# Optimization experiments

Hardware: AMD Instinct MI355X
Metric: run time of the kernel (lower is better)

The kernel has to match this reference:

```python
import jax, jax.numpy as jnp
import numpy as np

D_MODEL = 1024
NUM_HEADS = 16
D_K = D_MODEL // NUM_HEADS


def setup_inputs() -> dict:
    key = jax.random.key(0)
    ks = jax.random.split(key, 5)
    sd = np.sqrt(2.0 / (D_MODEL + D_MODEL))
    x = jax.random.normal(ks[0], (2, 2048, D_MODEL), dtype=jnp.float32)
    # weights stored as [out_features, in_features] like torch Linear
    w_q = jax.random.normal(ks[1], (D_MODEL, D_MODEL), dtype=jnp.float32) * (sd * sd)
    w_k = jax.random.normal(ks[2], (D_MODEL, D_MODEL), dtype=jnp.float32) * (sd * sd)
    w_v = jax.random.normal(ks[3], (D_MODEL, D_MODEL), dtype=jnp.float32) * (sd * sd)
    w_o = jax.random.normal(ks[4], (D_MODEL, D_MODEL), dtype=jnp.float32) * (sd * sd)
    return {"x": x, "w_q": w_q, "w_k": w_k, "w_v": w_v, "w_o": w_o}


def reference(x, w_q, w_k, w_v, w_o):
    B, S, D = x.shape
    H, Dk = NUM_HEADS, D_K
    # projections: x @ W.T
    q = (x @ w_q.T).reshape(B, S, H, Dk).transpose(0, 2, 1, 3)  # [B,H,S,Dk]
    k = (x @ w_k.T).reshape(B, S, H, Dk).transpose(0, 2, 1, 3)
    v = (x @ w_v.T).reshape(B, S, H, Dk).transpose(0, 2, 1, 3)
    scale = 1.0 / np.sqrt(Dk).astype(np.float32)
    scores = jnp.einsum('bhqd,bhkd->bhqk', q, k) * scale  # [B,H,S,S]
    causal = jnp.tril(jnp.ones((S, S), dtype=bool))
    scores = jnp.where(causal, scores, -jnp.inf)
    weights = jax.nn.softmax(scores, axis=-1)
    attn = jnp.einsum('bhqk,bhkd->bhqd', weights, v)  # [B,H,S,Dk]
    attn = attn.transpose(0, 2, 1, 3).reshape(B, S, D)
    return attn @ w_o.T
```

## Files before the change

### kernel.cpp

```cpp
#include <hip/hip_runtime.h>

typedef __attribute__((ext_vector_type(8))) short short8;
typedef __attribute__((ext_vector_type(4))) float f32x4;
typedef __attribute__((ext_vector_type(16))) float f32x16;
typedef __attribute__((ext_vector_type(2))) unsigned int u32x2;

#define DM 1024
#define SL 2048
#define NH 16
#define DKH 64
#define NB 2

__device__ __forceinline__ unsigned short f2bf(float f) {
    union { float f; unsigned int u; } a; a.f = f;
    unsigned int r = a.u + 0x7FFFu + ((a.u >> 16) & 1u);
    return (unsigned short)(r >> 16);
}

__device__ __forceinline__ void gl_lds16(const void* g, void* l) {
    __builtin_amdgcn_global_load_lds(
        (__attribute__((address_space(1))) void*)(g),
        (__attribute__((address_space(3))) void*)(l), 16, 0, 0);
}

__device__ __forceinline__ unsigned int cvtpk_bf16(float lo, float hi) {
    unsigned int r;
    asm("v_cvt_pk_bf16_f32 %0, %1, %2" : "=v"(r) : "v"(lo), "v"(hi));
    return r;
}

__device__ __forceinline__ void pl32swap(unsigned int &a, unsigned int &b) {
    u32x2 r = __builtin_amdgcn_permlane32_swap(a, b, false, false);
    a = r[0]; b = r[1];
}
__device__ __forceinline__ void pl32swapf(float &a, float &b) {
    unsigned int ua = __float_as_uint(a), ub = __float_as_uint(b);
    pl32swap(ua, ub);
    a = __uint_as_float(ua); b = __uint_as_float(ub);
}

__global__ __launch_bounds__(256) void convert_kernel(
    const float* __restrict__ x,  const float* __restrict__ wq,
    const float* __restrict__ wk, const float* __restrict__ wv,
    const float* __restrict__ wo,
    unsigned short* __restrict__ xb,  unsigned short* __restrict__ wqb,
    unsigned short* __restrict__ wkb, unsigned short* __restrict__ wvb,
    unsigned short* __restrict__ wob)
{
    const int NX = NB * SL * DM;
    const int NW = DM * DM;
    int t4 = (blockIdx.x * 256 + threadIdx.x) * 4;
    const float* src; unsigned short* dst; int off; float scale = 1.0f;
    if (t4 < NX)              { src = x;  dst = xb;  off = t4; }
    else if (t4 < NX + NW)    { src = wq; dst = wqb; off = t4 - NX; scale = 0.125f * 1.44269504088896f; }
    else if (t4 < NX + 2*NW)  { src = wk; dst = wkb; off = t4 - NX - NW; }
    else if (t4 < NX + 3*NW)  { src = wv; dst = wvb; off = t4 - NX - 2*NW; }
    else                      { src = wo; dst = wob; off = t4 - NX - 3*NW; }
    float4 v = *(const float4*)(src + off);
    unsigned long long p =
        (unsigned long long)f2bf(v.x * scale)
      | ((unsigned long long)f2bf(v.y * scale) << 16)
      | ((unsigned long long)f2bf(v.z * scale) << 32)
      | ((unsigned long long)f2bf(v.w * scale) << 48);
    *(unsigned long long*)(dst + off) = p;
}

template<int MODE>
__global__ __launch_bounds__(256) void gemm_bt(
    const unsigned short* __restrict__ A,
    const unsigned short* __restrict__ Bw,
    unsigned short* __restrict__ oq, unsigned short* __restrict__ ok,
    unsigned short* __restrict__ ov, float* __restrict__ of)
{
    __shared__ __align__(16) unsigned short As[128 * 64];
    __shared__ __align__(16) unsigned short Bs[128 * 64];
    const int tid  = threadIdx.x;
    const int lane = tid & 63;
    const int wave = tid >> 6;
    const int wm = (wave >> 1) * 64, wn = (wave & 1) * 64;
    const int bx = blockIdx.x, by = blockIdx.y;
    const int c    = lane & 15;
    const int kg16 = (lane >> 4) * 16;
    const int swz  = (c & 7) << 4;

    f32x4 acc[4][4];
    #pragma unroll
    for (int i = 0; i < 4; i++)
        #pragma unroll
        for (int j = 0; j < 4; j++) acc[i][j] = (f32x4){0.f, 0.f, 0.f, 0.f};

    const char* Ab = (const char*)A  + by * 128 * (DM * 2);
    const char* Bb = (const char*)Bw + bx * 128 * (DM * 2);

    for (int k0 = 0; k0 < DM; k0 += 64) {
        #pragma unroll
        for (int i = 0; i < 4; i++) {
            int o  = i * 4096 + tid * 16;
            int r  = o >> 7;
            int cb = o & 127;
            int src = r * (DM * 2) + k0 * 2 + (cb ^ ((r & 7) << 4));
            gl_lds16(Ab + src, (char*)As + o);
            gl_lds16(Bb + src, (char*)Bs + o);
        }
        __syncthreads();
        #pragma unroll
        for (int kk = 0; kk < 2; kk++) {
            short8 a[4], bfr[4];
            #pragma unroll
            for (int mi = 0; mi < 4; mi++)
                a[mi] = *(const short8*)((const char*)As
                        + (wm + mi * 16 + c) * 128 + ((kk * 64 + kg16) ^ swz));
            #pragma unroll
            for (int ni = 0; ni < 4; ni++)
                bfr[ni] = *(const short8*)((const char*)Bs
                        + (wn + ni * 16 + c) * 128 + ((kk * 64 + kg16) ^ swz));
            #pragma unroll
            for (int mi = 0; mi < 4; mi++)
                #pragma unroll
                for (int ni = 0; ni < 4; ni++)
                    acc[mi][ni] = __builtin_amdgcn_mfma_f32_16x16x32_bf16(
                        a[mi], bfr[ni], acc[mi][ni], 0, 0, 0);
        }
        __syncthreads();
    }

    const int r4 = (lane >> 4) * 4;
    if (MODE == 0) {
        const int mat = (bx * 128) >> 10;
        unsigned short* outb = (mat == 0) ? oq : (mat == 1) ? ok : ov;
        const int nb = bx * 128 - (mat << 10);
        #pragma unroll
        for (int mi = 0; mi < 4; mi++) {
            int m_g = by * 128 + wm + mi * 16 + r4;
            int b_  = m_g >> 11, s_ = m_g & 2047;
            #pragma unroll
            for (int ni = 0; ni < 4; ni++) {
                int n_l = nb + wn + ni * 16 + c;
                int h = n_l >> 6, dk = n_l & 63;
                #pragma unroll
                for (int j = 0; j < 4; j++)
                    outb[((b_ * NH + h) * SL + (s_ + j)) * DKH + dk] = f2bf(acc[mi][ni][j]);
            }
        }
    } else {
        #pragma unroll
        for (int mi = 0; mi < 4; mi++) {
            int m_g = by * 128 + wm + mi * 16 + r4;
            #pragma unroll
            for (int ni = 0; ni < 4; ni++) {
                int n_g = bx * 128 + wn + ni * 16 + c;
                #pragma unroll
                for (int j = 0; j < 4; j++)
                    of[(m_g + j) * DM + n_g] = acc[mi][ni][j];
            }
        }
    }
}

__global__ __launch_bounds__(256) void attn_kernel(
    const unsigned short* __restrict__ Q,
    const unsigned short* __restrict__ K,
    const unsigned short* __restrict__ V,
    unsigned short* __restrict__ O)
{
    __shared__ __align__(16) unsigned short Kl[2][128 * 64];
    __shared__ __align__(16) unsigned short Vt[2][16 * 64 * 8];
    const int tid = threadIdx.x, lane = tid & 63, wave = tid >> 6;
    const int ln31 = lane & 31, hi = lane >> 5;
    const int qt_raw = blockIdx.x >> 5;
    const int bh     = blockIdx.x & 31;
    const int qt = qt_raw < 8 ? qt_raw : 23 - qt_raw;
    const int b = bh >> 4, h = bh & 15;
    const int bhi = b * NH + h;
    const unsigned short* Qg = Q + bhi * (SL * DKH);
    const unsigned short* Kg = K + bhi * (SL * DKH);
    const unsigned short* Vg = V + bhi * (SL * DKH);
    const int qw = qt * 128 + wave * 32;
    const int ntiles = qt + 1;
    const int vd0 = (tid & 31) * 2, c0 = tid >> 5;

    short8 qf[4];
    #pragma unroll
    for (int ks = 0; ks < 4; ks++)
        qf[ks] = *(const short8*)&Qg[(qw + ln31) * DKH + ks * 16 + hi * 8];

    f32x16 OT0, OT1;
    #pragma unroll
    for (int r = 0; r < 16; r++) { OT0[r] = 0.f; OT1[r] = 0.f; }
    float mrun = -1e30f, ls = 0.f;

    unsigned int vreg[16];

    #pragma unroll
    for (int i = 0; i < 4; i++) {
        int s = i * 256 + tid;
        int kv = s >> 3;
        int k8 = (s & 7) ^ (kv & 7);
        gl_lds16((const char*)Kg + kv * 128 + k8 * 16, (char*)&Kl[0][0] + s * 16);
    }
    #pragma unroll
    for (int c2 = 0; c2 < 2; c2++)
        #pragma unroll
        for (int i = 0; i < 8; i++)
            vreg[c2 * 8 + i] = *(const unsigned int*)&Vg[((c0 + c2 * 8) * 8 + i) * DKH + vd0];

    for (int t = 0; t < ntiles; ++t) {
        const int buf = t & 1;
        const int kv0 = t * 128;
        #pragma unroll
        for (int c2 = 0; c2 < 2; c2++) {
            int chunk = c0 + c2 * 8;
            short8 sa, sb;
            #pragma unroll
            for (int i = 0; i < 8; i++) {
                unsigned int pr = vreg[c2 * 8 + i];
                sa[i] = (short)(pr & 0xFFFFu);
                sb[i] = (short)(pr >> 16);
            }
            *(short8*)&Vt[buf][(chunk * 64 + vd0) * 8]     = sa;
            *(short8*)&Vt[buf][(chunk * 64 + vd0 + 1) * 8] = sb;
        }
        __syncthreads();

        if (t + 1 < ntiles) {
            const int kv1 = (t + 1) * 128;
            #pragma unroll
            for (int i = 0; i < 4; i++) {
                int s = i * 256 + tid;
                int kv = s >> 3;
                int k8 = (s & 7) ^ (kv & 7);
                gl_lds16((const char*)Kg + (size_t)(kv1 + kv) * 128 + k8 * 16,
                         (char*)&Kl[buf ^ 1][0] + s * 16);
            }
            #pragma unroll
            for (int c2 = 0; c2 < 2; c2++)
                #pragma unroll
                for (int i = 0; i < 8; i++)
                    vreg[c2 * 8 + i] = *(const unsigned int*)&Vg[(size_t)(kv1 + (c0 + c2 * 8) * 8 + i) * DKH + vd0];
        }

        const char* kb = (const char*)&Kl[buf][0];
        const unsigned short* vb = &Vt[buf][0];
        #pragma unroll
        for (int hh = 0; hh < 2; hh++) {
            const int kvh = kv0 + hh * 64;
            if (kvh > qw + 31) break;

            f32x16 S0, S1;
            #pragma unroll
            for (int r = 0; r < 16; r++) { S0[r] = 0.f; S1[r] = 0.f; }
            #pragma unroll
            for (int ks = 0; ks < 4; ks++) {
                int ko = (ks * 32 + hi * 16) ^ ((ln31 & 7) << 4);
                short8 ka0 = *(const short8*)(kb + (hh * 64 + ln31) * 128 + ko);
                short8 ka1 = *(const short8*)(kb + (hh * 64 + 32 + ln31) * 128 + ko);
                S0 = __builtin_amdgcn_mfma_f32_32x32x16_bf16(ka0, qf[ks], S0, 0, 0, 0);
                S1 = __builtin_amdgcn_mfma_f32_32x32x16_bf16(ka1, qf[ks], S1, 0, 0, 0);
            }

            if (kvh + 63 > qw) {
                const int qrel0 = qw + ln31 - kvh - 4 * hi;
                const int qrel1 = qrel0 - 32;
                #pragma unroll
                for (int r = 0; r < 16; r++) {
                    const int ro = (r & 3) + 8 * (r >> 2);
                    if (ro > qrel0) S0[r] = -1e30f;
                    if (ro > qrel1) S1[r] = -1e30f;
                }
            }

            float mx = fmaxf(S0[0], S1[0]);
            #pragma unroll
            for (int r = 1; r < 16; r++) mx = fmaxf(mx, fmaxf(S0[r], S1[r]));
            float ma = mx, mb = mx;
            pl32swapf(ma, mb);
            float rm = fmaxf(ma, mb);

            if (__any(rm > mrun + 8.f)) {
                float nm = fmaxf(mrun, rm);
                float corr = exp2f(mrun - nm);
                mrun = nm; ls *= corr;
                #pragma unroll
                for (int r = 0; r < 16; r++) { OT0[r] *= corr; OT1[r] *= corr; }
            }

            float psum = 0.f;
            #pragma unroll
            for (int r = 0; r < 16; r++) {
                S0[r] = exp2f(S0[r] - mrun); psum += S0[r];
                S1[r] = exp2f(S1[r] - mrun); psum += S1[r];
            }
            ls += psum;

            short8 pf[4];
            {
                unsigned int wa, wb, wc, wd;
                wa = cvtpk_bf16(S0[0], S0[1]);   wb = cvtpk_bf16(S0[4], S0[5]);
                pl32swap(wa, wb);
                wc = cvtpk_bf16(S0[2], S0[3]);   wd = cvtpk_bf16(S0[6], S0[7]);
                pl32swap(wc, wd);
                union { unsigned int u[4]; short8 s; } w0 = {{wa, wc, wb, wd}};
                pf[0] = w0.s;

                wa = cvtpk_bf16(S0[8], S0[9]);   wb = cvtpk_bf16(S0[12], S0[13]);
                pl32swap(wa, wb);
                wc = cvtpk_bf16(S0[10], S0[11]); wd = cvtpk_bf16(S0[14], S0[15]);
                pl32swap(wc, wd);
                union { unsigned int u[4]; short8 s; } w1 = {{wa, wc, wb, wd}};
                pf[1] = w1.s;

                wa = cvtpk_bf16(S1[0], S1[1]);   wb = cvtpk_bf16(S1[4], S1[5]);
                pl32swap(wa, wb);
                wc = cvtpk_bf16(S1[2], S1[3]);   wd = cvtpk_bf16(S1[6], S1[7]);
                pl32swap(wc, wd);
                union { unsigned int u[4]; short8 s; } w2 = {{wa, wc, wb, wd}};
                pf[2] = w2.s;

                wa = cvtpk_bf16(S1[8], S1[9]);   wb = cvtpk_bf16(S1[12], S1[13]);
                pl32swap(wa, wb);
                wc = cvtpk_bf16(S1[10], S1[11]); wd = cvtpk_bf16(S1[14], S1[15]);
                pl32swap(wc, wd);
                union { unsigned int u[4]; short8 s; } w3 = {{wa, wc, wb, wd}};
                pf[3] = w3.s;
            }

            #pragma unroll
            for (int ks2 = 0; ks2 < 4; ks2++) {
                int slot = (hh * 8 + ks2 * 2 + hi) * 64;
                short8 va0 = *(const short8*)&vb[(slot + ln31) * 8];
                short8 va1 = *(const short8*)&vb[(slot + 32 + ln31) * 8];
                OT0 = __builtin_amdgcn_mfma_f32_32x32x16_bf16(va0, pf[ks2], OT0, 0, 0, 0);
                OT1 = __builtin_amdgcn_mfma_f32_32x32x16_bf16(va1, pf[ks2], OT1, 0, 0, 0);
            }
        }
    }

    float la = ls, lb = ls;
    pl32swapf(la, lb);
    float inv = 1.0f / (la + lb);
    const int qrow = qw + ln31;
    const size_t base = (size_t)(b * SL + qrow) * DM + h * DKH;
    #pragma unroll
    for (int r = 0; r < 16; r++) {
        const int d0 = (r & 3) + 8 * (r >> 2) + 4 * hi;
        O[base + d0]      = f2bf(OT0[r] * inv);
        O[base + 32 + d0] = f2bf(OT1[r] * inv);
    }
}

extern "C" void kernel_launch(void* const* d_in, const int* in_sizes, int n_in,
                              void* d_out, int out_size, void* d_ws, size_t ws_size,
                              hipStream_t stream)
{
    const float* x  = (const float*)d_in[0];
    const float* wq = (const float*)d_in[1];
    const float* wk = (const float*)d_in[2];
    const float* wv = (const float*)d_in[3];
    const float* wo = (const float*)d_in[4];
    char* ws = (char*)d_ws;
    unsigned short* xb  = (unsigned short*)(ws);
    unsigned short* wqb = (unsigned short*)(ws + (8ll  << 20));
    unsigned short* wkb = (unsigned short*)(ws + (10ll << 20));
    unsigned short* wvb = (unsigned short*)(ws + (12ll << 20));
    unsigned short* wob = (unsigned short*)(ws + (14ll << 20));
    unsigned short* Qb  = (unsigned short*)(ws + (16ll << 20));
    unsigned short* Kb  = (unsigned short*)(ws + (24ll << 20));
    unsigned short* Vb  = (unsigned short*)(ws + (32ll << 20));
    unsigned short* Abf = (unsigned short*)(ws + (40ll << 20));
    float* out = (float*)d_out;

    convert_kernel<<<dim3(8192), dim3(256), 0, stream>>>(
        x, wq, wk, wv, wo, xb, wqb, wkb, wvb, wob);

    gemm_bt<0><<<dim3(24, 32), dim3(256), 0, stream>>>(
        xb, wqb, Qb, Kb, Vb, (float*)nullptr);

    attn_kernel<<<dim3(512), dim3(256), 0, stream>>>(Qb, Kb, Vb, Abf);

    gemm_bt<1><<<dim3(8, 32), dim3(256), 0, stream>>>(
        Abf, wob, nullptr, nullptr, nullptr, out);
}
```

Before: 120.2 us.

## Shrink attention blocks to 64-query tiles with 2 waves and 64-key tiles

The attention kernel moves from 256-thread blocks covering 128 queries to 128-thread blocks covering 64 queries, with 64-key tiles, so the grid doubles to 1024 blocks. Causal load balancing becomes a four-way pairing of query tiles. The inner two-half loop goes away and only the final tile is masked. It also adds s_setprio around the MFMA sections and uses the raw exp2 builtin. The aim is better occupancy and load balance, at the cost of more K/V reloads across blocks and more barriers per unit of work.

```diff
diff --git a/kernel.cpp b/kernel.cpp
--- a/kernel.cpp
+++ b/kernel.cpp
@@ -157,25 +157,29 @@
     }
 }
 
-__global__ __launch_bounds__(256) void attn_kernel(
+__global__ __launch_bounds__(128) void attn_kernel(
     const unsigned short* __restrict__ Q,
     const unsigned short* __restrict__ K,
     const unsigned short* __restrict__ V,
     unsigned short* __restrict__ O)
 {
-    __shared__ __align__(16) unsigned short Kl[2][128 * 64];
-    __shared__ __align__(16) unsigned short Vt[2][16 * 64 * 8];
+    __shared__ __align__(16) unsigned short Kl[2][64 * 64];
+    __shared__ __align__(16) unsigned short Vt[2][8 * 64 * 8];
     const int tid = threadIdx.x, lane = tid & 63, wave = tid >> 6;
     const int ln31 = lane & 31, hi = lane >> 5;
     const int qt_raw = blockIdx.x >> 5;
     const int bh     = blockIdx.x & 31;
-    const int qt = qt_raw < 8 ? qt_raw : 23 - qt_raw;
+    const int quad = qt_raw >> 3;
+    const int qt = (quad == 0) ? qt_raw
+                 : (quad == 1) ? (23 - qt_raw)
+                 : (quad == 2) ? (qt_raw + 8)
+                 :               (47 - qt_raw);
     const int b = bh >> 4, h = bh & 15;
     const int bhi = b * NH + h;
     const unsigned short* Qg = Q + bhi * (SL * DKH);
     const unsigned short* Kg = K + bhi * (SL * DKH);
     const unsigned short* Vg = V + bhi * (SL * DKH);
-    const int qw = qt * 128 + wave * 32;
+    const int qw = qt * 64 + wave * 32;
     const int ntiles = qt + 1;
     const int vd0 = (tid & 31) * 2, c0 = tid >> 5;
 
@@ -193,7 +197,7 @@
 
     #pragma unroll
     for (int i = 0; i < 4; i++) {
-        int s = i * 256 + tid;
+        int s = i * 128 + tid;
         int kv = s >> 3;
         int k8 = (s & 7) ^ (kv & 7);
         gl_lds16((const char*)Kg + kv * 128 + k8 * 16, (char*)&Kl[0][0] + s * 16);
@@ -202,14 +206,14 @@
     for (int c2 = 0; c2 < 2; c2++)
         #pragma unroll
         for (int i = 0; i < 8; i++)
-            vreg[c2 * 8 + i] = *(const unsigned int*)&Vg[((c0 + c2 * 8) * 8 + i) * DKH + vd0];
+            vreg[c2 * 8 + i] = *(const unsigned int*)&Vg[((c0 + 4 * c2) * 8 + i) * DKH + vd0];
 
     for (int t = 0; t < ntiles; ++t) {
         const int buf = t & 1;
-        const int kv0 = t * 128;
+        const int kv0 = t * 64;
         #pragma unroll
         for (int c2 = 0; c2 < 2; c2++) {
-            int chunk = c0 + c2 * 8;
+            int chunk = c0 + 4 * c2;
             short8 sa, sb;
             #pragma unroll
             for (int i = 0; i < 8; i++) {
@@ -223,10 +227,10 @@
         __syncthreads();
 
         if (t + 1 < ntiles) {
-            const int kv1 = (t + 1) * 128;
+            const int kv1 = (t + 1) * 64;
             #pragma unroll
             for (int i = 0; i < 4; i++) {
-                int s = i * 256 + tid;
+                int s = i * 128 + tid;
                 int kv = s >> 3;
                 int k8 = (s & 7) ^ (kv & 7);
                 gl_lds16((const char*)Kg + (size_t)(kv1 + kv) * 128 + k8 * 16,
@@ -236,103 +240,102 @@
             for (int c2 = 0; c2 < 2; c2++)
                 #pragma unroll
                 for (int i = 0; i < 8; i++)
-                    vreg[c2 * 8 + i] = *(const unsigned int*)&Vg[(size_t)(kv1 + (c0 + c2 * 8) * 8 + i) * DKH + vd0];
+                    vreg[c2 * 8 + i] = *(const unsigned int*)&Vg[(size_t)(kv1 + (c0 + 4 * c2) * 8 + i) * DKH + vd0];
         }
 
         const char* kb = (const char*)&Kl[buf][0];
         const unsigned short* vb = &Vt[buf][0];
-        #pragma unroll
-        for (int hh = 0; hh < 2; hh++) {
-            const int kvh = kv0 + hh * 64;
-            if (kvh > qw + 31) break;
-
-            f32x16 S0, S1;
-            #pragma unroll
-            for (int r = 0; r < 16; r++) { S0[r] = 0.f; S1[r] = 0.f; }
-            #pragma unroll
-            for (int ks = 0; ks < 4; ks++) {
-                int ko = (ks * 32 + hi * 16) ^ ((ln31 & 7) << 4);
-                short8 ka0 = *(const short8*)(kb + (hh * 64 + ln31) * 128 + ko);
-                short8 ka1 = *(const short8*)(kb + (hh * 64 + 32 + ln31) * 128 + ko);
-                S0 = __builtin_amdgcn_mfma_f32_32x32x16_bf16(ka0, qf[ks], S0, 0, 0, 0);
-                S1 = __builtin_amdgcn_mfma_f32_32x32x16_bf16(ka1, qf[ks], S1, 0, 0, 0);
-            }
-
-            if (kvh + 63 > qw) {
-                const int qrel0 = qw + ln31 - kvh - 4 * hi;
-                const int qrel1 = qrel0 - 32;
-                #pragma unroll
-                for (int r = 0; r < 16; r++) {
-                    const int ro = (r & 3) + 8 * (r >> 2);
-                    if (ro > qrel0) S0[r] = -1e30f;
-                    if (ro > qrel1) S1[r] = -1e30f;
-                }
-            }
-
-            float mx = fmaxf(S0[0], S1[0]);
-            #pragma unroll
-            for (int r = 1; r < 16; r++) mx = fmaxf(mx, fmaxf(S0[r], S1[r]));
-            float ma = mx, mb = mx;
-            pl32swapf(ma, mb);
-            float rm = fmaxf(ma, mb);
-
-            if (__any(rm > mrun + 8.f)) {
-                float nm = fmaxf(mrun, rm);
-                float corr = exp2f(mrun - nm);
-                mrun = nm; ls *= corr;
-                #pragma unroll
-                for (int r = 0; r < 16; r++) { OT0[r] *= corr; OT1[r] *= corr; }
-            }
-
-            float psum = 0.f;
+
+        f32x16 S0, S1;
+        #pragma unroll
+        for (int r = 0; r < 16; r++) { S0[r] = 0.f; S1[r] = 0.f; }
+        __builtin_amdgcn_s_setprio(1);
+        #pragma unroll
+        for (int ks = 0; ks < 4; ks++) {
+            int ko = (ks * 32 + hi * 16) ^ ((ln31 & 7) << 4);
+            short8 ka0 = *(const short8*)(kb + ln31 * 128 + ko);
+            short8 ka1 = *(const short8*)(kb + (32 + ln31) * 128 + ko);
+            S0 = __builtin_amdgcn_mfma_f32_32x32x16_bf16(ka0, qf[ks], S0, 0, 0, 0);
+            S1 = __builtin_amdgcn_mfma_f32_32x32x16_bf16(ka1, qf[ks], S1, 0, 0, 0);
+        }
+        __builtin_amdgcn_s_setprio(0);
+
+        if (t == ntiles - 1) {
+            const int qrel0 = qw + ln31 - kv0 - 4 * hi;
+            const int qrel1 = qrel0 - 32;
             #pragma unroll
             for (int r = 0; r < 16; r++) {
-                S0[r] = exp2f(S0[r] - mrun); psum += S0[r];
-                S1[r] = exp2f(S1[r] - mrun); psum += S1[r];
-            }
-            ls += psum;
-
-            short8 pf[4];
-            {
-                unsigned int wa, wb, wc, wd;
-                wa = cvtpk_bf16(S0[0], S0[1]);   wb = cvtpk_bf16(S0[4], S0[5]);
-                pl32swap(wa, wb);
-                wc = cvtpk_bf16(S0[2], S0[3]);   wd = cvtpk_bf16(S0[6], S0[7]);
-                pl32swap(wc, wd);
-                union { unsigned int u[4]; short8 s; } w0 = {{wa, wc, wb, wd}};
-                pf[0] = w0.s;
-
-                wa = cvtpk_bf16(S0[8], S0[9]);   wb = cvtpk_bf16(S0[12], S0[13]);
-                pl32swap(wa, wb);
-                wc = cvtpk_bf16(S0[10], S0[11]); wd = cvtpk_bf16(S0[14], S0[15]);
-                pl32swap(wc, wd);
-                union { unsigned int u[4]; short8 s; } w1 = {{wa, wc, wb, wd}};
-                pf[1] = w1.s;
-
-                wa = cvtpk_bf16(S1[0], S1[1]);   wb = cvtpk_bf16(S1[4], S1[5]);
-                pl32swap(wa, wb);
-                wc = cvtpk_bf16(S1[2], S1[3]);   wd = cvtpk_bf16(S1[6], S1[7]);
-                pl32swap(wc, wd);
-                union { unsigned int u[4]; short8 s; } w2 = {{wa, wc, wb, wd}};
-                pf[2] = w2.s;
-
-                wa = cvtpk_bf16(S1[8], S1[9]);   wb = cvtpk_bf16(S1[12], S1[13]);
-                pl32swap(wa, wb);
-                wc = cvtpk_bf16(S1[10], S1[11]); wd = cvtpk_bf16(S1[14], S1[15]);
-                pl32swap(wc, wd);
-                union { unsigned int u[4]; short8 s; } w3 = {{wa, wc, wb, wd}};
-                pf[3] = w3.s;
-            }
-
-            #pragma unroll
-            for (int ks2 = 0; ks2 < 4; ks2++) {
-                int slot = (hh * 8 + ks2 * 2 + hi) * 64;
-                short8 va0 = *(const short8*)&vb[(slot + ln31) * 8];
-                short8 va1 = *(const short8*)&vb[(slot + 32 + ln31) * 8];
-                OT0 = __builtin_amdgcn_mfma_f32_32x32x16_bf16(va0, pf[ks2], OT0, 0, 0, 0);
-                OT1 = __builtin_amdgcn_mfma_f32_32x32x16_bf16(va1, pf[ks2], OT1, 0, 0, 0);
-            }
-        }
+                const int ro = (r & 3) + 8 * (r >> 2);
+                if (ro > qrel0) S0[r] = -1e30f;
+                if (ro > qrel1) S1[r] = -1e30f;
+            }
+        }
+
+        float mx = fmaxf(S0[0], S1[0]);
+        #pragma unroll
+        for (int r = 1; r < 16; r++) mx = fmaxf(mx, fmaxf(S0[r], S1[r]));
+        float ma = mx, mb = mx;
+        pl32swapf(ma, mb);
+        float rm = fmaxf(ma, mb);
+
+        if (__any(rm > mrun + 8.f)) {
+            float nm = fmaxf(mrun, rm);
+            float corr = __builtin_amdgcn_exp2f(mrun - nm);
+            mrun = nm; ls *= corr;
+            #pragma unroll
+            for (int r = 0; r < 16; r++) { OT0[r] *= corr; OT1[r] *= corr; }
+        }
+
+        float psum = 0.f;
+        #pragma unroll
+        for (int r = 0; r < 16; r++) {
+            S0[r] = __builtin_amdgcn_exp2f(S0[r] - mrun); psum += S0[r];
+            S1[r] = __builtin_amdgcn_exp2f(S1[r] - mrun); psum += S1[r];
+        }
+        ls += psum;
+
+        short8 pf[4];
+        {
+            unsigned int wa, wb, wc, wd;
+            wa = cvtpk_bf16(S0[0], S0[1]);   wb = cvtpk_bf16(S0[4], S0[5]);
+            pl32swap(wa, wb);
+            wc = cvtpk_bf16(S0[2], S0[3]);   wd = cvtpk_bf16(S0[6], S0[7]);
+            pl32swap(wc, wd);
+            union { unsigned int u[4]; short8 s; } w0 = {{wa, wc, wb, wd}};
+            pf[0] = w0.s;
+
+            wa = cvtpk_bf16(S0[8], S0[9]);   wb = cvtpk_bf16(S0[12], S0[13]);
+            pl32swap(wa, wb);
+            wc = cvtpk_bf16(S0[10], S0[11]); wd = cvtpk_bf16(S0[14], S0[15]);
+            pl32swap(wc, wd);
+            union { unsigned int u[4]; short8 s; } w1 = {{wa, wc, wb, wd}};
+            pf[1] = w1.s;
+
+            wa = cvtpk_bf16(S1[0], S1[1]);   wb = cvtpk_bf16(S1[4], S1[5]);
+            pl32swap(wa, wb);
+            wc = cvtpk_bf16(S1[2], S1[3]);   wd = cvtpk_bf16(S1[6], S1[7]);
+            pl32swap(wc, wd);
+            union { unsigned int u[4]; short8 s; } w2 = {{wa, wc, wb, wd}};
+            pf[2] = w2.s;
+
+            wa = cvtpk_bf16(S1[8], S1[9]);   wb = cvtpk_bf16(S1[12], S1[13]);
+            pl32swap(wa, wb);
+            wc = cvtpk_bf16(S1[10], S1[11]); wd = cvtpk_bf16(S1[14], S1[15]);
+            pl32swap(wc, wd);
+            union { unsigned int u[4]; short8 s; } w3 = {{wa, wc, wb, wd}};
+            pf[3] = w3.s;
+        }
+
+        __builtin_amdgcn_s_setprio(1);
+        #pragma unroll
+        for (int ks2 = 0; ks2 < 4; ks2++) {
+            int slot = (ks2 * 2 + hi) * 64;
+            short8 va0 = *(const short8*)&vb[(slot + ln31) * 8];
+            short8 va1 = *(const short8*)&vb[(slot + 32 + ln31) * 8];
+            OT0 = __builtin_amdgcn_mfma_f32_32x32x16_bf16(va0, pf[ks2], OT0, 0, 0, 0);
+            OT1 = __builtin_amdgcn_mfma_f32_32x32x16_bf16(va1, pf[ks2], OT1, 0, 0, 0);
+        }
+        __builtin_amdgcn_s_setprio(0);
     }
 
     float la = ls, lb = ls;
@@ -375,7 +378,7 @@
     gemm_bt<0><<<dim3(24, 32), dim3(256), 0, stream>>>(
         xb, wqb, Qb, Kb, Vb, (float*)nullptr);
 
-    attn_kernel<<<dim3(512), dim3(256), 0, stream>>>(Qb, Kb, Vb, Abf);
+    attn_kernel<<<dim3(1024), dim3(128), 0, stream>>>(Qb, Kb, Vb, Abf);
 
     gemm_bt<1><<<dim3(8, 32), dim3(256), 0, stream>>>(
         Abf, wob, nullptr, nullptr, nullptr, out);
```

New measurement: 120.8 us. No clear change (+0.5%).
